# Kernel optimization log

Hardware: AMD Instinct MI355X
Metric: run time of the kernel (lower is better)

The kernel has to match this reference:

```python
import jax, jax.numpy as jnp
import numpy as np

B = 32768
D_VIS, D_LANG, D_STATE = 256, 128, 128
D_MODEL, N_EXP, TOP_K = 512, 8, 2
D_IN = D_VIS + D_LANG + D_STATE
EPS = 1e-5

def _gelu(x):
    # torch nn.GELU default = exact erf form
    return jax.nn.gelu(x, approximate=False)

def _ln(x, g, b):
    mu = x.mean(-1, keepdims=True)
    var = ((x - mu) ** 2).mean(-1, keepdims=True)
    return (x - mu) / jnp.sqrt(var + EPS) * g + b

def setup_inputs() -> dict:
    key = jax.random.key(0)
    ks = jax.random.split(key, 16)
    f32 = jnp.float32
    def w(k, shape, fan_in):
        return jax.random.normal(k, shape, dtype=f32) * (1.0 / np.sqrt(fan_in))
    return {
        "vis":   jax.random.normal(ks[0], (B, D_VIS), dtype=f32),
        "lang":  jax.random.normal(ks[1], (B, D_LANG), dtype=f32),
        "state": jax.random.normal(ks[2], (B, D_STATE), dtype=f32),
        # fusion: Linear(D_IN, D_MODEL) + LayerNorm + GELU
        "Wf": w(ks[3], (D_IN, D_MODEL), D_IN),
        "bf": jnp.zeros((D_MODEL,), f32),
        "gf": jnp.ones((D_MODEL,), f32),
        "betaf": jnp.zeros((D_MODEL,), f32),
        # gate (bias-free); random instead of torch's zeros-init so routing is non-degenerate
        "Wg": w(ks[4], (D_MODEL, N_EXP), D_MODEL),
        # stacked expert params: d -> 2d -> d -> d, residual LayerNorm
        "W1": w(ks[5], (N_EXP, D_MODEL, 2 * D_MODEL), D_MODEL),
        "b1": jnp.zeros((N_EXP, 2 * D_MODEL), f32),
        "W2": w(ks[6], (N_EXP, 2 * D_MODEL, D_MODEL), 2 * D_MODEL),
        "b2": jnp.zeros((N_EXP, D_MODEL), f32),
        "W3": w(ks[7], (N_EXP, D_MODEL, D_MODEL), D_MODEL),
        "b3": jnp.zeros((N_EXP, D_MODEL), f32),
        "ge": jnp.ones((N_EXP, D_MODEL), f32),
        "be": jnp.zeros((N_EXP, D_MODEL), f32),
    }

def reference(vis, lang, state, Wf, bf, gf, betaf, Wg, W1, b1, W2, b2, W3, b3, ge, be):
    # fusion projection  [B, D_IN] -> [B, D_MODEL]
    x = _gelu(_ln(jnp.concatenate([vis, lang, state], axis=-1) @ Wf + bf, gf, betaf))
    logits = x @ Wg                              # [B, E]
    all_probs = jax.nn.softmax(logits, axis=-1)  # [B, E]
    top_vals, top_idx = jax.lax.top_k(logits, TOP_K)   # [B, K]
    top_w = jax.nn.softmax(top_vals, axis=-1)          # [B, K]
    # per-(token, expert) combine weight: sum_k top_w[b,k] * [top_idx[b,k]==e]
    onehot = jax.nn.one_hot(top_idx, N_EXP, dtype=x.dtype)   # [B, K, E]
    combine = (onehot * top_w[..., None]).sum(axis=1)        # [B, E]
    out = jnp.zeros_like(x)
    for e in range(N_EXP):  # small fixed expert count; dense compute, sparse combine
        h = _gelu(x @ W1[e] + b1[e])
        h = _gelu(h @ W2[e] + b2[e])
        h = h @ W3[e] + b3[e]
        y = _ln(x + h, ge[e], be[e])            # Expert: ln(x + net(x))
        out = out + combine[:, e:e + 1] * y
    # load-balancing aux loss (counts carry no gradient, as in torch scatter_add of ones)
    counts = onehot.sum(axis=(0, 1))            # [E]
    f_i = counts / (B * TOP_K)
    lb_loss = N_EXP * jnp.sum(f_i * all_probs.mean(axis=0))
    return out, lb_loss
```

## Files before the change

### kernel.cpp

```cpp
#include <hip/hip_runtime.h>
#include <math.h>

typedef __bf16     bf16x8 __attribute__((ext_vector_type(8)));
typedef _Float16   f16x8  __attribute__((ext_vector_type(8)));
typedef float      f32x4  __attribute__((ext_vector_type(4)));
typedef unsigned short u16x8 __attribute__((ext_vector_type(8)));

#define DEVI __device__ __forceinline__
constexpr int B_TOK = 32768;
constexpr int MAXT  = 520;

DEVI unsigned short f2bf(float f){
  unsigned int u = __builtin_bit_cast(unsigned int, f);
  u += 0x7fffu + ((u >> 16) & 1u);
  return (unsigned short)(u >> 16);
}
DEVI float bf2f(unsigned short b){
  return __builtin_bit_cast(float, (unsigned int)b << 16);
}
DEVI float gelu_fast(float x){
  float z = fabsf(x) * 0.70710678118654752f;
  float t = __builtin_amdgcn_rcpf(1.f + 0.3275911f * z);
  float p = t*(0.254829592f + t*(-0.284496736f + t*(1.421413741f + t*(-1.453152027f + t*1.061405429f))));
  float e = __expf(-z * z);
  float erfz = 1.f - p * e;
  float s = copysignf(erfz, x);
  return 0.5f * x * (1.f + s);
}
DEVI void load16_lds(const void* g, void* l){
  __builtin_amdgcn_global_load_lds(
      (const __attribute__((address_space(1))) unsigned int*)g,
      (__attribute__((address_space(3))) unsigned int*)l, 16, 0, 0);
}
DEVI float wredsum(float v){
#pragma unroll
  for (int off = 32; off > 0; off >>= 1) v += __shfl_xor(v, off, 64);
  return v;
}

__global__ void transpose_cast_bf16_k(const float* __restrict__ src, unsigned short* __restrict__ dst,
                                      int R, int C){
  __shared__ float tile[32][33];
  size_t base = (size_t)blockIdx.z * R * C;
  int c0 = blockIdx.x * 32, r0 = blockIdx.y * 32;
  for (int i = threadIdx.y; i < 32; i += 8)
    tile[i][threadIdx.x] = src[base + (size_t)(r0 + i) * C + c0 + threadIdx.x];
  __syncthreads();
  for (int i = threadIdx.y; i < 32; i += 8)
    dst[base + (size_t)(c0 + i) * R + r0 + threadIdx.x] = f2bf(tile[threadIdx.x][i]);
}

__global__ void transpose_split_f16_k(const float* __restrict__ src, unsigned short* __restrict__ dh,
                                      unsigned short* __restrict__ dl, int R, int C){
  __shared__ float tile[32][33];
  int c0 = blockIdx.x * 32, r0 = blockIdx.y * 32;
  for (int i = threadIdx.y; i < 32; i += 8)
    tile[i][threadIdx.x] = src[(size_t)(r0 + i) * C + c0 + threadIdx.x];
  __syncthreads();
  for (int i = threadIdx.y; i < 32; i += 8){
    float f = tile[threadIdx.x][i];
    _Float16 h = (_Float16)f;
    _Float16 l = (_Float16)(f - (float)h);
    size_t o = (size_t)(c0 + i) * R + r0 + threadIdx.x;
    dh[o] = __builtin_bit_cast(unsigned short, h);
    dl[o] = __builtin_bit_cast(unsigned short, l);
  }
}

__global__ __launch_bounds__(256, 2) void gemm_fusion_f16split(
    const float* __restrict__ vis, const float* __restrict__ lang, const float* __restrict__ state,
    const unsigned short* __restrict__ Wh, const unsigned short* __restrict__ Wl,
    const float* __restrict__ bias, float* __restrict__ Xpre)
{
  constexpr int K = 512, N = 512;
  __shared__ alignas(16) unsigned short smemF[32768];
  unsigned short* AhS = smemF;
  unsigned short* AlS = smemF + 8192;
  unsigned short* BhS = smemF + 16384;
  unsigned short* BlS = smemF + 24576;
  const int tid = threadIdx.x;
  const int row_s = tid >> 3, col_s = (tid & 7) * 8;
  const int swz = (row_s & 7) << 3;
  const unsigned short *pbh[4], *pbl[4];
  int arow[4];
#pragma unroll
  for (int i = 0; i < 4; ++i){
    arow[i] = blockIdx.x * 128 + i * 32 + row_s;
    size_t br = (size_t)(blockIdx.y * 128 + i * 32 + row_s) * K + (col_s ^ swz);
    pbh[i] = Wh + br; pbl[i] = Wl + br;
  }
  const int w = tid >> 6, lane = tid & 63;
  const int wr = (w >> 1) * 64, wc = (w & 1) * 64;
  const int lm = lane & 15, lk8 = (lane >> 4) * 8;
  const int fxor = (lm & 7) << 3;
  f32x4 acc[4][4] = {};
  for (int k0 = 0; k0 < K; k0 += 64){
#pragma unroll
    for (int i = 0; i < 4; ++i){
      load16_lds(pbh[i] + k0, &BhS[i*2048 + tid*8]);
      load16_lds(pbl[i] + k0, &BlS[i*2048 + tid*8]);
    }
    int col = k0 + col_s;
#pragma unroll
    for (int i = 0; i < 4; ++i){
      const float* src;
      if (col < 256)      src = vis   + (size_t)arow[i] * 256 + col;
      else if (col < 384) src = lang  + (size_t)arow[i] * 128 + (col - 256);
      else                src = state + (size_t)arow[i] * 128 + (col - 384);
      float4 a = *(const float4*)src, b = *(const float4*)(src + 4);
      float f[8] = {a.x, a.y, a.z, a.w, b.x, b.y, b.z, b.w};
      u16x8 hh, ll;
#pragma unroll
      for (int j = 0; j < 8; ++j){
        _Float16 h = (_Float16)f[j];
        _Float16 l = (_Float16)(f[j] - (float)h);
        hh[j] = __builtin_bit_cast(unsigned short, h);
        ll[j] = __builtin_bit_cast(unsigned short, l);
      }
      *(u16x8*)&AhS[i*2048 + row_s*64 + (col_s ^ swz)] = hh;
      *(u16x8*)&AlS[i*2048 + row_s*64 + (col_s ^ swz)] = ll;
    }
    __syncthreads();
#pragma unroll
    for (int kk = 0; kk < 64; kk += 32){
      f16x8 fah[4], fal[4], fbh[4], fbl[4];
#pragma unroll
      for (int m = 0; m < 4; ++m){
        int ro = (wr + m*16 + lm) * 64 + ((kk + lk8) ^ fxor);
        fah[m] = *(const f16x8*)&AhS[ro];
        fal[m] = *(const f16x8*)&AlS[ro];
      }
#pragma unroll
      for (int n = 0; n < 4; ++n){
        int ro = (wc + n*16 + lm) * 64 + ((kk + lk8) ^ fxor);
        fbh[n] = *(const f16x8*)&BhS[ro];
        fbl[n] = *(const f16x8*)&BlS[ro];
      }
#pragma unroll
      for (int m = 0; m < 4; ++m)
#pragma unroll
        for (int n = 0; n < 4; ++n){
          acc[m][n] = __builtin_amdgcn_mfma_f32_16x16x32_f16(fah[m], fbh[n], acc[m][n], 0, 0, 0);
          acc[m][n] = __builtin_amdgcn_mfma_f32_16x16x32_f16(fal[m], fbh[n], acc[m][n], 0, 0, 0);
          acc[m][n] = __builtin_amdgcn_mfma_f32_16x16x32_f16(fah[m], fbl[n], acc[m][n], 0, 0, 0);
        }
    }
    __syncthreads();
  }
  float* Cs = (float*)smemF;
  const int lk4 = (lane >> 4) * 4;
#pragma unroll
  for (int n = 0; n < 4; ++n){
    float bv = bias[blockIdx.y * 128 + wc + n*16 + lm];
#pragma unroll
    for (int m = 0; m < 4; ++m)
#pragma unroll
      for (int r = 0; r < 4; ++r){
        int rr = wr + m*16 + lk4 + r;
        Cs[rr * 128 + ((wc + n*16 + lm) ^ ((rr & 7) << 2))] = acc[m][n][r] + bv;
      }
  }
  __syncthreads();
#pragma unroll
  for (int j = 0; j < 16; ++j){
    int r = j*8 + (tid >> 5), c = (tid & 31) * 4;
    float4 v = *(const float4*)&Cs[r*128 + (c ^ ((r & 7) << 2))];
    *(float4*)&Xpre[(size_t)(blockIdx.x*128 + r) * N + blockIdx.y*128 + c] = v;
  }
}

__global__ void build_tiles_k(const int* __restrict__ cnt, int* __restrict__ nTiles,
                              int* __restrict__ tileE, int* __restrict__ tileR0,
                              int* __restrict__ rowBase){
  if (threadIdx.x == 0 && blockIdx.x == 0){
    int t = 0;
    for (int e = 0; e < 8; ++e){
      int c = cnt[e]; c = c < 0 ? 0 : (c > B_TOK ? B_TOK : c);
      rowBase[e] = t * 128;
      for (int r = 0; r < c; r += 128){ tileE[t] = e; tileR0[t] = r; ++t; }
    }
    nTiles[0] = t;
    for (int i = t; i < MAXT; ++i){ tileE[i] = 0; tileR0[i] = 0; }
  }
}

template<int K, int N, bool GATHER, bool GELU_ACT, bool GLOBAL_ROW>
__global__ __launch_bounds__(256, 2) void egemm_k(
    const unsigned short* __restrict__ A, const int* __restrict__ rowlist,
    const int* __restrict__ cnt, const int* __restrict__ nTilesP,
    const int* __restrict__ tileE, const int* __restrict__ tileR0, int chunkBase,
    const unsigned short* __restrict__ W, const float* __restrict__ bias,
    unsigned short* __restrict__ Cout)
{
  const int t = chunkBase + blockIdx.y;
  if (t >= nTilesP[0]) return;
  const int e = tileE[t], r0 = tileR0[t];
  int rows = cnt[e] - r0; rows = rows > 128 ? 128 : rows;
  __shared__ alignas(16) unsigned short smem[16384];
  unsigned short* As = smem;
  unsigned short* Bs = smem + 8192;
  const int tid = threadIdx.x;
  const int row_s = tid >> 3, col_s = (tid & 7) * 8;
  const int swz = (row_s & 7) << 3;
  const unsigned short *pa[4], *pb[4];
#pragma unroll
  for (int i = 0; i < 4; ++i){
    int ir = i * 32 + row_s;
    size_t arow;
    if (GATHER){
      int rr = ir < rows ? ir : rows - 1;
      arow = (size_t)rowlist[(size_t)e * B_TOK + r0 + rr];
    } else {
      arow = (size_t)blockIdx.y * 128 + ir;
    }
    pa[i] = A + arow * K + (col_s ^ swz);
    pb[i] = W + (size_t)e * ((size_t)N * K) + (size_t)(blockIdx.x * 128 + ir) * K + (col_s ^ swz);
  }
  const int w = tid >> 6, lane = tid & 63;
  const int wr = (w >> 1) * 64, wc = (w & 1) * 64;
  const int lm = lane & 15, lk8 = (lane >> 4) * 8;
  const int fxor = (lm & 7) << 3;
  f32x4 acc[4][4] = {};
  for (int k0 = 0; k0 < K; k0 += 64){
#pragma unroll
    for (int i = 0; i < 4; ++i) load16_lds(pa[i] + k0, &As[i*2048 + tid*8]);
#pragma unroll
    for (int i = 0; i < 4; ++i) load16_lds(pb[i] + k0, &Bs[i*2048 + tid*8]);
    __syncthreads();
#pragma unroll
    for (int kk = 0; kk < 64; kk += 32){
      bf16x8 a[4], b[4];
#pragma unroll
      for (int m = 0; m < 4; ++m)
        a[m] = *(const bf16x8*)&As[(wr + m*16 + lm)*64 + ((kk + lk8) ^ fxor)];
#pragma unroll
      for (int n = 0; n < 4; ++n)
        b[n] = *(const bf16x8*)&Bs[(wc + n*16 + lm)*64 + ((kk + lk8) ^ fxor)];
#pragma unroll
      for (int m = 0; m < 4; ++m)
#pragma unroll
        for (int n = 0; n < 4; ++n)
          acc[m][n] = __builtin_amdgcn_mfma_f32_16x16x32_bf16(a[m], b[n], acc[m][n], 0, 0, 0);
    }
    __syncthreads();
  }
  unsigned short* Cs = smem;
  const int lk4 = (lane >> 4) * 4;
#pragma unroll
  for (int n = 0; n < 4; ++n){
    float bv = bias[(size_t)e * N + blockIdx.x * 128 + wc + n*16 + lm];
#pragma unroll
    for (int m = 0; m < 4; ++m)
#pragma unroll
      for (int r = 0; r < 4; ++r){
        float v = acc[m][n][r] + bv;
        if (GELU_ACT) v = gelu_fast(v);
        int rr = wr + m*16 + lk4 + r;
        Cs[rr * 128 + ((wc + n*16 + lm) ^ ((rr & 7) << 3))] = f2bf(v);
      }
  }
  __syncthreads();
  const size_t outTile = GLOBAL_ROW ? (size_t)t * 128 : (size_t)blockIdx.y * 128;
#pragma unroll
  for (int j = 0; j < 8; ++j){
    int r = j*16 + (tid >> 4), c = (tid & 15) * 8;
    if (r < rows){
      u16x8 v = *(const u16x8*)&Cs[r*128 + (c ^ ((r & 7) << 3))];
      *(u16x8*)&Cout[(outTile + r) * N + blockIdx.x*128 + c] = v;
    }
  }
}

__global__ __launch_bounds__(256) void ln_gelu_gate_k(
    const float* __restrict__ Xpre, const float* __restrict__ gf,
    const float* __restrict__ betaf, const float* __restrict__ Wg,
    unsigned short* __restrict__ Xbf, int* __restrict__ cursor,
    float* __restrict__ probs_sum, int* __restrict__ rowlist,
    int* __restrict__ TS, float* __restrict__ TW)
{
  __shared__ float s_probs[8];
  __shared__ int s_cnt[8], s_base[8];
  __shared__ int s_e0[16], s_e1[16], s_r0[16], s_r1[16];
  __shared__ float s_w0[16], s_w1[16];
  const int tid = threadIdx.x, wv = tid >> 6, lane = tid & 63;
  if (tid < 8){ s_probs[tid] = 0.f; s_cnt[tid] = 0; }
  __syncthreads();
  float gg[8], bb[8], wg[8][8];
  {
    const float4* gp = (const float4*)(gf + lane * 8);
    const float4* bp = (const float4*)(betaf + lane * 8);
    float4 g0 = gp[0], g1 = gp[1], c0 = bp[0], c1 = bp[1];
    gg[0]=g0.x; gg[1]=g0.y; gg[2]=g0.z; gg[3]=g0.w; gg[4]=g1.x; gg[5]=g1.y; gg[6]=g1.z; gg[7]=g1.w;
    bb[0]=c0.x; bb[1]=c0.y; bb[2]=c0.z; bb[3]=c0.w; bb[4]=c1.x; bb[5]=c1.y; bb[6]=c1.z; bb[7]=c1.w;
#pragma unroll
    for (int j = 0; j < 8; ++j){
      const float4* wrow = (const float4*)(Wg + (size_t)(lane * 8 + j) * 8);
      float4 w0 = wrow[0], w1 = wrow[1];
      wg[j][0]=w0.x; wg[j][1]=w0.y; wg[j][2]=w0.z; wg[j][3]=w0.w;
      wg[j][4]=w1.x; wg[j][5]=w1.y; wg[j][6]=w1.z; wg[j][7]=w1.w;
    }
  }
#pragma unroll
  for (int it = 0; it < 4; ++it){
    const int tloc = wv * 4 + it;
    const int row = blockIdx.x * 16 + tloc;
    const float* xp = Xpre + (size_t)row * 512 + lane * 8;
    float4 v0 = *(const float4*)xp, v1 = *(const float4*)(xp + 4);
    float v[8] = {v0.x, v0.y, v0.z, v0.w, v1.x, v1.y, v1.z, v1.w};
    float s1 = 0.f, s2 = 0.f;
#pragma unroll
    for (int j = 0; j < 8; ++j){ s1 += v[j]; s2 += v[j]*v[j]; }
    {
      float sel = (lane & 1) ? s1 : s2;
      float r = __shfl_xor(sel, 1, 64);
      float tt = ((lane & 1) ? s2 : s1) + r;
#pragma unroll
      for (int off = 2; off < 64; off <<= 1) tt += __shfl_xor(tt, off, 64);
      float other = __shfl_xor(tt, 1, 64);
      s1 = (lane & 1) ? other : tt;
      s2 = (lane & 1) ? tt : other;
    }
    const float mu  = s1 * (1.f / 512.f);
    const float var = s2 * (1.f / 512.f) - mu * mu;
    const float inv = 1.f / sqrtf(var + 1e-5f);
    float o[8];
#pragma unroll
    for (int j = 0; j < 8; ++j)
      o[j] = gelu_fast((v[j] - mu) * inv * gg[j] + bb[j]);
    u16x8 ob;
#pragma unroll
    for (int j = 0; j < 8; ++j) ob[j] = f2bf(o[j]);
    *(u16x8*)(Xbf + (size_t)row * 512 + lane * 8) = ob;
    float acc[8] = {0.f,0.f,0.f,0.f,0.f,0.f,0.f,0.f};
#pragma unroll
    for (int j = 0; j < 8; ++j)
#pragma unroll
      for (int e = 0; e < 8; ++e) acc[e] += o[j] * wg[j][e];
    float v4[4], v2[2], v1f;
#pragma unroll
    for (int i = 0; i < 4; ++i){
      float sel = (lane & 1) ? acc[i] : acc[i+4];
      float r = __shfl_xor(sel, 1, 64);
      v4[i] = ((lane & 1) ? acc[i+4] : acc[i]) + r;
    }
#pragma unroll
    for (int i = 0; i < 2; ++i){
      float sel = (lane & 2) ? v4[i] : v4[i+2];
      float r = __shfl_xor(sel, 2, 64);
      v2[i] = ((lane & 2) ? v4[i+2] : v4[i]) + r;
    }
    {
      float sel = (lane & 4) ? v2[0] : v2[1];
      float r = __shfl_xor(sel, 4, 64);
      v1f = ((lane & 4) ? v2[1] : v2[0]) + r;
    }
#pragma unroll
    for (int off = 8; off < 64; off <<= 1) v1f += __shfl_xor(v1f, off, 64);
    float lg[8];
#pragma unroll
    for (int e = 0; e < 8; ++e){
      int src = (lane & 56) | ((e >> 2) & 1) | (((e >> 1) & 1) << 1) | ((e & 1) << 2);
      lg[e] = __shfl(v1f, src, 64);
    }
    float mx = lg[0];
#pragma unroll
    for (int e = 1; e < 8; ++e) mx = fmaxf(mx, lg[e]);
    float pe[8], ps = 0.f;
#pragma unroll
    for (int e = 0; e < 8; ++e){ pe[e] = __expf(lg[e] - mx); ps += pe[e]; }
    float invp = 1.f / ps;
    int i1 = 0;
#pragma unroll
    for (int e = 1; e < 8; ++e) if (lg[e] > lg[i1]) i1 = e;
    int i2 = (i1 == 0) ? 1 : 0;
#pragma unroll
    for (int e = 0; e < 8; ++e) if (e != i1 && lg[e] > lg[i2]) i2 = e;
    float wA = 1.f / (1.f + __expf(lg[i2] - lg[i1]));
    float wB = 1.f - wA;
    if (lane == 0){
#pragma unroll
      for (int e = 0; e < 8; ++e) atomicAdd(&s_probs[e], pe[e] * invp);
      int r0 = atomicAdd(&s_cnt[i1], 1);
      int r1 = atomicAdd(&s_cnt[i2], 1);
      s_e0[tloc] = i1; s_r0[tloc] = r0; s_w0[tloc] = wA;
      s_e1[tloc] = i2; s_r1[tloc] = r1; s_w1[tloc] = wB;
    }
  }
  __syncthreads();
  if (tid < 8){
    s_base[tid] = atomicAdd(&cursor[tid], s_cnt[tid]);
    atomicAdd(&probs_sum[tid], s_probs[tid]);
  }
  __syncthreads();
  if (tid < 16){
    int t = blockIdx.x * 16 + tid;
    int e0 = s_e0[tid], e1 = s_e1[tid];
    int p0 = s_base[e0] + s_r0[tid], p1 = s_base[e1] + s_r1[tid];
    rowlist[(size_t)e0 * B_TOK + p0] = t;
    rowlist[(size_t)e1 * B_TOK + p1] = t;
    TS[t*2]   = (e0 << 15) | p0;  TW[t*2]   = s_w0[tid];
    TS[t*2+1] = (e1 << 15) | p1;  TW[t*2+1] = s_w1[tid];
  }
}

__global__ void lb_k(const int* __restrict__ cursor, const float* __restrict__ probs, float* __restrict__ dst){
  if (threadIdx.x == 0 && blockIdx.x == 0){
    float acc = 0.f;
    for (int e = 0; e < 8; ++e)
      acc += ((float)cursor[e] / (float)(B_TOK * 2)) * (probs[e] / (float)B_TOK);
    dst[0] = 8.f * acc;
  }
}

__global__ __launch_bounds__(256) void combine_k(
    const unsigned short* __restrict__ Xbf, const unsigned short* __restrict__ H3F,
    const int* __restrict__ TS, const float* __restrict__ TW,
    const int* __restrict__ rowBase, const float* __restrict__ ge,
    const float* __restrict__ be, float* __restrict__ out)
{
  const int tok = blockIdx.x * 4 + (threadIdx.x >> 6);
  const int lane = threadIdx.x & 63;
  u16x8 xb = *(const u16x8*)(Xbf + (size_t)tok * 512 + lane * 8);
  float x[8];
#pragma unroll
  for (int j = 0; j < 8; ++j) x[j] = bf2f(xb[j]);
  float o[8] = {0.f,0.f,0.f,0.f,0.f,0.f,0.f,0.f};
#pragma unroll
  for (int kslot = 0; kslot < 2; ++kslot){
    int sl = TS[tok*2 + kslot];
    float wgt = TW[tok*2 + kslot];
    int e = sl >> 15, p = sl & 32767;
    size_t hrow = (size_t)(rowBase[e] + p);
    u16x8 hb = *(const u16x8*)(H3F + hrow * 512 + lane * 8);
    float s[8];
#pragma unroll
    for (int j = 0; j < 8; ++j) s[j] = x[j] + bf2f(hb[j]);
    float sm = 0.f;
#pragma unroll
    for (int j = 0; j < 8; ++j) sm += s[j];
    sm = wredsum(sm);
    float mu = sm * (1.f / 512.f);
    float q = 0.f;
#pragma unroll
    for (int j = 0; j < 8; ++j){ float d = s[j] - mu; q += d * d; }
    q = wredsum(q);
    float inv = 1.f / sqrtf(q * (1.f / 512.f) + 1e-5f);
    const float4* gp = (const float4*)(ge + (size_t)e * 512 + lane * 8);
    const float4* bp = (const float4*)(be + (size_t)e * 512 + lane * 8);
    float4 g0 = gp[0], g1 = gp[1], c0 = bp[0], c1 = bp[1];
    float gg[8] = {g0.x,g0.y,g0.z,g0.w,g1.x,g1.y,g1.z,g1.w};
    float bb[8] = {c0.x,c0.y,c0.z,c0.w,c1.x,c1.y,c1.z,c1.w};
#pragma unroll
    for (int j = 0; j < 8; ++j)
      o[j] += wgt * ((s[j]-mu)*inv*gg[j] + bb[j]);
  }
  float* op = out + (size_t)tok * 512 + lane * 8;
  *(float4*)op       = make_float4(o[0], o[1], o[2], o[3]);
  *(float4*)(op + 4) = make_float4(o[4], o[5], o[6], o[7]);
}

extern "C" void kernel_launch(void* const* d_in, const int* in_sizes, int n_in,
                              void* d_out, int out_size, void* d_ws, size_t ws_size,
                              hipStream_t stream)
{
  (void)in_sizes; (void)n_in; (void)out_size;
  const float* vis   = (const float*)d_in[0];
  const float* lang  = (const float*)d_in[1];
  const float* state = (const float*)d_in[2];
  const float* Wf    = (const float*)d_in[3];
  const float* bf    = (const float*)d_in[4];
  const float* gf    = (const float*)d_in[5];
  const float* betaf = (const float*)d_in[6];
  const float* Wg    = (const float*)d_in[7];
  const float* W1    = (const float*)d_in[8];
  const float* b1    = (const float*)d_in[9];
  const float* W2    = (const float*)d_in[10];
  const float* b2    = (const float*)d_in[11];
  const float* W3    = (const float*)d_in[12];
  const float* b3    = (const float*)d_in[13];
  const float* ge    = (const float*)d_in[14];
  const float* be    = (const float*)d_in[15];

  char* ws = (char*)d_ws;
  size_t off = 0;
  auto alloc = [&](size_t n){ size_t o = off; off += (n + 255) & ~(size_t)255; return o; };

  unsigned short* WFH  = (unsigned short*)(ws + alloc((size_t)512*512*2));
  unsigned short* WFL  = (unsigned short*)(ws + alloc((size_t)512*512*2));
  unsigned short* W1T  = (unsigned short*)(ws + alloc((size_t)8*1024*512*2));
  unsigned short* W2T  = (unsigned short*)(ws + alloc((size_t)8*512*1024*2));
  unsigned short* W3T  = (unsigned short*)(ws + alloc((size_t)8*512*512*2));
  unsigned short* XBF  = (unsigned short*)(ws + alloc((size_t)B_TOK*512*2));
  int*            RLIST= (int*)(ws + alloc((size_t)8*B_TOK*4));
  int*            TS   = (int*)(ws + alloc((size_t)B_TOK*2*4));
  float*          TW   = (float*)(ws + alloc((size_t)B_TOK*2*4));
  size_t cnt_off = alloc(256);
  int*            CNT  = (int*)(ws + cnt_off);
  float*          PROBS= (float*)(ws + alloc(256));
  int*            NT   = (int*)(ws + alloc(64));
  int*            RB   = (int*)(ws + alloc(64));
  int*            TE   = (int*)(ws + alloc(MAXT*4));
  int*            TR   = (int*)(ws + alloc(MAXT*4));
  unsigned short* H3F  = (unsigned short*)(ws + alloc((size_t)MAXT*128*512*2));

  const size_t perTile = (size_t)128*1024*2 + (size_t)128*512*2;
  size_t remain = (ws_size > off) ? (ws_size - off) : 0;
  int tch, nch;
  size_t need2 = (size_t)260 * perTile, need4 = (size_t)B_TOK*512*4;
  if (remain >= need2 && need2 >= need4){ tch = 260; nch = 2; }
  else { tch = 130; nch = 4; }
  size_t regB = alloc(need2 > need4 ? (nch == 2 ? need2 : need4) : need4);
  float*          XPRE = (float*)(ws + regB);
  unsigned short* H1   = (unsigned short*)(ws + regB);
  unsigned short* H2   = H1 + (size_t)tch*128*1024;

  hipMemsetAsync(ws + cnt_off, 0, 512, stream);

  transpose_split_f16_k<<<dim3(16,16,1), dim3(32,8), 0, stream>>>(Wf, WFH, WFL, 512, 512);
  transpose_cast_bf16_k<<<dim3(32,16,8), dim3(32,8), 0, stream>>>(W1, W1T, 512, 1024);
  transpose_cast_bf16_k<<<dim3(16,32,8), dim3(32,8), 0, stream>>>(W2, W2T, 1024, 512);
  transpose_cast_bf16_k<<<dim3(16,16,8), dim3(32,8), 0, stream>>>(W3, W3T, 512, 512);
  gemm_fusion_f16split<<<dim3(256,4), 256, 0, stream>>>(vis, lang, state, WFH, WFL, bf, XPRE);
  ln_gelu_gate_k<<<B_TOK/16, 256, 0, stream>>>(XPRE, gf, betaf, Wg, XBF, CNT, PROBS, RLIST, TS, TW);
  build_tiles_k<<<1, 64, 0, stream>>>(CNT, NT, TE, TR, RB);
  lb_k<<<1, 64, 0, stream>>>(CNT, PROBS, ((float*)d_out) + (size_t)B_TOK*512);

  for (int c = 0; c < nch; ++c){
    int cb = c * tch;
    egemm_k<512, 1024, true,  true,  false><<<dim3(8, tch), 256, 0, stream>>>(
        XBF, RLIST, CNT, NT, TE, TR, cb, W1T, b1, H1);
    egemm_k<1024, 512, false, true,  false><<<dim3(4, tch), 256, 0, stream>>>(
        H1,  RLIST, CNT, NT, TE, TR, cb, W2T, b2, H2);
    egemm_k<512,  512, false, false, true ><<<dim3(4, tch), 256, 0, stream>>>(
        H2,  RLIST, CNT, NT, TE, TR, cb, W3T, b3, H3F);
  }
  combine_k<<<B_TOK/4, 256, 0, stream>>>(XBF, H3F, TS, TW, RB, ge, be, (float*)d_out);
}
```

Baseline: 516.4 us.

## Replace global atomic routing cursors with per-block counts, scan, and placement kernel

The gating kernel no longer does global atomicAdds on expert cursors and probability sums. It writes per-block expert counts and probabilities plus a packed per-token routing record. A single-block scan kernel computes per-block bases, expert totals, the tile list and the load-balancing loss, and a placement kernel then writes the row lists and combine slots. This makes the routing order deterministic and removes atomic contention and a memset, at the cost of an extra launch and a serial single-block scan. The Xpre loads are also issued up front to improve memory-level parallelism.

```diff
diff --git a/kernel.cpp b/kernel.cpp
--- a/kernel.cpp
+++ b/kernel.cpp
@@ -9,6 +9,7 @@
 #define DEVI __device__ __forceinline__
 constexpr int B_TOK = 32768;
 constexpr int MAXT  = 520;
+constexpr int NBLK  = B_TOK / 16;
 
 DEVI unsigned short f2bf(float f){
   unsigned int u = __builtin_bit_cast(unsigned int, f);
@@ -169,21 +170,6 @@
   }
 }
 
-__global__ void build_tiles_k(const int* __restrict__ cnt, int* __restrict__ nTiles,
-                              int* __restrict__ tileE, int* __restrict__ tileR0,
-                              int* __restrict__ rowBase){
-  if (threadIdx.x == 0 && blockIdx.x == 0){
-    int t = 0;
-    for (int e = 0; e < 8; ++e){
-      int c = cnt[e]; c = c < 0 ? 0 : (c > B_TOK ? B_TOK : c);
-      rowBase[e] = t * 128;
-      for (int r = 0; r < c; r += 128){ tileE[t] = e; tileR0[t] = r; ++t; }
-    }
-    nTiles[0] = t;
-    for (int i = t; i < MAXT; ++i){ tileE[i] = 0; tileR0[i] = 0; }
-  }
-}
-
 template<int K, int N, bool GATHER, bool GELU_ACT, bool GLOBAL_ROW>
 __global__ __launch_bounds__(256, 2) void egemm_k(
     const unsigned short* __restrict__ A, const int* __restrict__ rowlist,
@@ -274,14 +260,13 @@
 __global__ __launch_bounds__(256) void ln_gelu_gate_k(
     const float* __restrict__ Xpre, const float* __restrict__ gf,
     const float* __restrict__ betaf, const float* __restrict__ Wg,
-    unsigned short* __restrict__ Xbf, int* __restrict__ cursor,
-    float* __restrict__ probs_sum, int* __restrict__ rowlist,
-    int* __restrict__ TS, float* __restrict__ TW)
+    unsigned short* __restrict__ Xbf, int* __restrict__ PK,
+    int* __restrict__ BlockCnt, float* __restrict__ BlockProbs)
 {
   __shared__ float s_probs[8];
-  __shared__ int s_cnt[8], s_base[8];
-  __shared__ int s_e0[16], s_e1[16], s_r0[16], s_r1[16];
-  __shared__ float s_w0[16], s_w1[16];
+  __shared__ int s_cnt[8];
+  __shared__ int s_pk[16];
+  __shared__ float s_w[16];
   const int tid = threadIdx.x, wv = tid >> 6, lane = tid & 63;
   if (tid < 8){ s_probs[tid] = 0.f; s_cnt[tid] = 0; }
   __syncthreads();
@@ -300,13 +285,20 @@
       wg[j][4]=w1.x; wg[j][5]=w1.y; wg[j][6]=w1.z; wg[j][7]=w1.w;
     }
   }
+  float4 vv[4][2];
+#pragma unroll
+  for (int it = 0; it < 4; ++it){
+    const int row = blockIdx.x * 16 + wv * 4 + it;
+    const float* xp = Xpre + (size_t)row * 512 + lane * 8;
+    vv[it][0] = *(const float4*)xp;
+    vv[it][1] = *(const float4*)(xp + 4);
+  }
 #pragma unroll
   for (int it = 0; it < 4; ++it){
     const int tloc = wv * 4 + it;
     const int row = blockIdx.x * 16 + tloc;
-    const float* xp = Xpre + (size_t)row * 512 + lane * 8;
-    float4 v0 = *(const float4*)xp, v1 = *(const float4*)(xp + 4);
-    float v[8] = {v0.x, v0.y, v0.z, v0.w, v1.x, v1.y, v1.z, v1.w};
+    float v[8] = {vv[it][0].x, vv[it][0].y, vv[it][0].z, vv[it][0].w,
+                  vv[it][1].x, vv[it][1].y, vv[it][1].z, vv[it][1].w};
     float s1 = 0.f, s2 = 0.f;
 #pragma unroll
     for (int j = 0; j < 8; ++j){ s1 += v[j]; s2 += v[j]*v[j]; }
@@ -376,40 +368,97 @@
 #pragma unroll
     for (int e = 0; e < 8; ++e) if (e != i1 && lg[e] > lg[i2]) i2 = e;
     float wA = 1.f / (1.f + __expf(lg[i2] - lg[i1]));
-    float wB = 1.f - wA;
     if (lane == 0){
 #pragma unroll
       for (int e = 0; e < 8; ++e) atomicAdd(&s_probs[e], pe[e] * invp);
       int r0 = atomicAdd(&s_cnt[i1], 1);
       int r1 = atomicAdd(&s_cnt[i2], 1);
-      s_e0[tloc] = i1; s_r0[tloc] = r0; s_w0[tloc] = wA;
-      s_e1[tloc] = i2; s_r1[tloc] = r1; s_w1[tloc] = wB;
+      s_pk[tloc] = i1 | (r0 << 3) | (i2 << 8) | (r1 << 16);
+      s_w[tloc] = wA;
     }
   }
   __syncthreads();
   if (tid < 8){
-    s_base[tid] = atomicAdd(&cursor[tid], s_cnt[tid]);
-    atomicAdd(&probs_sum[tid], s_probs[tid]);
-  }
-  __syncthreads();
+    BlockCnt[blockIdx.x * 8 + tid] = s_cnt[tid];
+    BlockProbs[blockIdx.x * 8 + tid] = s_probs[tid];
+  }
   if (tid < 16){
     int t = blockIdx.x * 16 + tid;
-    int e0 = s_e0[tid], e1 = s_e1[tid];
-    int p0 = s_base[e0] + s_r0[tid], p1 = s_base[e1] + s_r1[tid];
-    rowlist[(size_t)e0 * B_TOK + p0] = t;
-    rowlist[(size_t)e1 * B_TOK + p1] = t;
-    TS[t*2]   = (e0 << 15) | p0;  TW[t*2]   = s_w0[tid];
-    TS[t*2+1] = (e1 << 15) | p1;  TW[t*2+1] = s_w1[tid];
-  }
-}
-
-__global__ void lb_k(const int* __restrict__ cursor, const float* __restrict__ probs, float* __restrict__ dst){
-  if (threadIdx.x == 0 && blockIdx.x == 0){
+    PK[2*t]   = s_pk[tid];
+    PK[2*t+1] = __builtin_bit_cast(int, s_w[tid]);
+  }
+}
+
+__global__ __launch_bounds__(256) void scan_k(
+    const int* __restrict__ BlockCnt, const float* __restrict__ BlockProbs,
+    int* __restrict__ BlockBase, int* __restrict__ CNT, int* __restrict__ nTiles,
+    int* __restrict__ tileE, int* __restrict__ tileR0, int* __restrict__ rowBase,
+    float* __restrict__ lbOut)
+{
+  __shared__ int sScan[256];
+  __shared__ float sF[256];
+  __shared__ int sTot[8];
+  __shared__ float sProbTot[8];
+  const int tid = threadIdx.x;
+  for (int e = 0; e < 8; ++e){
+    int local[8]; int sum = 0;
+#pragma unroll
+    for (int j = 0; j < 8; ++j){ local[j] = BlockCnt[(tid*8 + j)*8 + e]; sum += local[j]; }
+    float fsum = 0.f;
+#pragma unroll
+    for (int j = 0; j < 8; ++j) fsum += BlockProbs[(tid*8 + j)*8 + e];
+    sScan[tid] = sum; sF[tid] = fsum;
+    __syncthreads();
+    for (int off = 1; off < 256; off <<= 1){
+      int add = (tid >= off) ? sScan[tid - off] : 0;
+      __syncthreads();
+      sScan[tid] += add;
+      __syncthreads();
+    }
+    for (int off = 128; off > 0; off >>= 1){
+      if (tid < off) sF[tid] += sF[tid + off];
+      __syncthreads();
+    }
+    int base = (tid == 0) ? 0 : sScan[tid - 1];
+    int run = base;
+#pragma unroll
+    for (int j = 0; j < 8; ++j){ BlockBase[(tid*8 + j)*8 + e] = run; run += local[j]; }
+    if (tid == 0){ sTot[e] = sScan[255]; sProbTot[e] = sF[0]; }
+    __syncthreads();
+  }
+  if (tid == 0){
+    int t = 0;
+    for (int e = 0; e < 8; ++e){
+      int c = sTot[e]; c = c < 0 ? 0 : (c > B_TOK ? B_TOK : c);
+      CNT[e] = c;
+      rowBase[e] = t * 128;
+      for (int r = 0; r < c; r += 128){ tileE[t] = e; tileR0[t] = r; ++t; }
+    }
+    nTiles[0] = t;
+    for (int i = t; i < MAXT; ++i){ tileE[i] = 0; tileR0[i] = 0; }
     float acc = 0.f;
     for (int e = 0; e < 8; ++e)
-      acc += ((float)cursor[e] / (float)(B_TOK * 2)) * (probs[e] / (float)B_TOK);
-    dst[0] = 8.f * acc;
-  }
+      acc += ((float)sTot[e] / (float)(B_TOK * 2)) * (sProbTot[e] / (float)B_TOK);
+    lbOut[0] = 8.f * acc;
+  }
+}
+
+__global__ __launch_bounds__(256) void place_k(
+    const int* __restrict__ PK, const int* __restrict__ BlockBase,
+    int* __restrict__ rowlist, int* __restrict__ TS, float* __restrict__ TW)
+{
+  const int t = blockIdx.x * 256 + threadIdx.x;
+  int pk = PK[2*t];
+  float w0 = __builtin_bit_cast(float, PK[2*t+1]);
+  int e0 = pk & 7, r0 = (pk >> 3) & 31;
+  int e1 = (pk >> 8) & 7, r1 = (pk >> 16) & 31;
+  int blk = t >> 4;
+  int p0 = BlockBase[blk*8 + e0] + r0;
+  int p1 = BlockBase[blk*8 + e1] + r1;
+  rowlist[(size_t)e0 * B_TOK + p0] = t;
+  rowlist[(size_t)e1 * B_TOK + p1] = t;
+  TS[2*t]   = (e0 << 15) | p0;  TW[2*t]   = w0;
+  TS[2*t+1] = (e1 << 15) | p1;  TW[2*t+1] = 1.f - w0;
 }
 
 __global__ __launch_bounds__(256) void combine_k(
@@ -494,9 +543,11 @@
   int*            RLIST= (int*)(ws + alloc((size_t)8*B_TOK*4));
   int*            TS   = (int*)(ws + alloc((size_t)B_TOK*2*4));
   float*          TW   = (float*)(ws + alloc((size_t)B_TOK*2*4));
-  size_t cnt_off = alloc(256);
-  int*            CNT  = (int*)(ws + cnt_off);
-  float*          PROBS= (float*)(ws + alloc(256));
+  int*            PK   = (int*)(ws + alloc((size_t)B_TOK*2*4));
+  int*            BCNT = (int*)(ws + alloc((size_t)NBLK*8*4));
+  float*          BPROB= (float*)(ws + alloc((size_t)NBLK*8*4));
+  int*            BBASE= (int*)(ws + alloc((size_t)NBLK*8*4));
+  int*            CNT  = (int*)(ws + alloc(64));
   int*            NT   = (int*)(ws + alloc(64));
   int*            RB   = (int*)(ws + alloc(64));
   int*            TE   = (int*)(ws + alloc(MAXT*4));
@@ -514,16 +565,15 @@
   unsigned short* H1   = (unsigned short*)(ws + regB);
   unsigned short* H2   = H1 + (size_t)tch*128*1024;
 
-  hipMemsetAsync(ws + cnt_off, 0, 512, stream);
-
   transpose_split_f16_k<<<dim3(16,16,1), dim3(32,8), 0, stream>>>(Wf, WFH, WFL, 512, 512);
   transpose_cast_bf16_k<<<dim3(32,16,8), dim3(32,8), 0, stream>>>(W1, W1T, 512, 1024);
   transpose_cast_bf16_k<<<dim3(16,32,8), dim3(32,8), 0, stream>>>(W2, W2T, 1024, 512);
   transpose_cast_bf16_k<<<dim3(16,16,8), dim3(32,8), 0, stream>>>(W3, W3T, 512, 512);
   gemm_fusion_f16split<<<dim3(256,4), 256, 0, stream>>>(vis, lang, state, WFH, WFL, bf, XPRE);
-  ln_gelu_gate_k<<<B_TOK/16, 256, 0, stream>>>(XPRE, gf, betaf, Wg, XBF, CNT, PROBS, RLIST, TS, TW);
-  build_tiles_k<<<1, 64, 0, stream>>>(CNT, NT, TE, TR, RB);
-  lb_k<<<1, 64, 0, stream>>>(CNT, PROBS, ((float*)d_out) + (size_t)B_TOK*512);
+  ln_gelu_gate_k<<<NBLK, 256, 0, stream>>>(XPRE, gf, betaf, Wg, XBF, PK, BCNT, BPROB);
+  scan_k<<<1, 256, 0, stream>>>(BCNT, BPROB, BBASE, CNT, NT, TE, TR, RB,
+                                ((float*)d_out) + (size_t)B_TOK*512);
+  place_k<<<B_TOK/256, 256, 0, stream>>>(PK, BBASE, RLIST, TS, TW);
 
   for (int c = 0; c < nch; ++c){
     int cb = c * tch;
```

Measured after the change: 546.9 us. 1.06x slower.
